# Kernel tuning notes

Hardware: AMD Instinct MI355X
Metric: run time of the kernel (lower is better)

Reference implementation:

```python
import jax, jax.numpy as jnp
import numpy as np

SEQ, N_NODES, N_EDGES = 64, 4096, 65536
IN_CH, HID, OUT = 128, 256, 256  # conv1: IN->2*HID, conv2: 2*HID->HID; HID==OUT required by the model


def setup_inputs() -> dict:
    key = jax.random.key(0)
    ks = jax.random.split(key, 10)
    s = 0.05
    return {
        "x": jax.random.normal(ks[0], (SEQ, N_NODES, IN_CH), jnp.float32),
        "edge_index": jax.random.randint(ks[1], (SEQ, 2, N_EDGES), 0, N_NODES),
        "W1l": jax.random.normal(ks[2], (IN_CH, 2 * HID), jnp.float32) * s,
        "b1l": jnp.zeros((2 * HID,), jnp.float32),
        "W1r": jax.random.normal(ks[3], (IN_CH, 2 * HID), jnp.float32) * s,
        "W2l": jax.random.normal(ks[4], (2 * HID, HID), jnp.float32) * s,
        "b2l": jnp.zeros((HID,), jnp.float32),
        "W2r": jax.random.normal(ks[5], (2 * HID, HID), jnp.float32) * s,
        "Wih": jax.random.normal(ks[6], (3 * OUT, HID), jnp.float32) * s,
        "Whh": jax.random.normal(ks[7], (3 * OUT, OUT), jnp.float32) * s,
        "bih": jnp.zeros((3 * OUT,), jnp.float32),
        "bhh": jnp.zeros((3 * OUT,), jnp.float32),
        "timestamp": 4,
        "n_samples": 8,
    }


def _sage(xt, src, dst, Wl, bl, Wr):
    # PyG SAGEConv: lin_l(mean-aggregated neighbor msgs) + lin_r(x); bias on lin_l only
    agg = jax.ops.segment_sum(xt[src], dst, num_segments=N_NODES)
    deg = jax.ops.segment_sum(jnp.ones((src.shape[0],), xt.dtype), dst, num_segments=N_NODES)
    agg = agg / jnp.maximum(deg, 1.0)[:, None]
    return agg @ Wl + bl + xt @ Wr


def _cpc_indices(seq_len, timestamp, n_samples):
    neg_dist = seq_len // 6
    end = seq_len - n_samples - neg_dist - timestamp + 2
    start = seq_len // 8 if seq_len // 8 < end else 0
    t_samples = np.arange(start, end)
    off = np.zeros((timestamp, n_samples), np.int32)
    for i in range(1, timestamp + 1):
        off[i - 1, 0] = i  # positive sample
        for j in range(1, n_samples):
            off[i - 1, j] = i + neg_dist + j - 1  # negatives
    return t_samples, off


def reference(x, edge_index, W1l, b1l, W1r, W2l, b2l, W2r, Wih, Whh, bih, bhh, timestamp, n_samples):
    def per_t(xt, ei):
        src, dst = ei[0], ei[1]
        h = jax.nn.relu(_sage(xt, src, dst, W1l, b1l, W1r))  # dropout(p=0.5) is identity in eval
        h = _sage(h, src, dst, W2l, b2l, W2r)
        return h.max(axis=0)  # global_max_pool over the single graph

    z = jax.vmap(per_t)(x, edge_index)  # [SEQ, HID]

    # torch GRU receives [1, t+1, H] seq-major => a single GRU-cell step per element, h0 = 0
    gi = z @ Wih.T + bih  # [SEQ, 3*OUT]
    r = jax.nn.sigmoid(gi[:, :OUT] + bhh[:OUT])
    u = jax.nn.sigmoid(gi[:, OUT:2 * OUT] + bhh[OUT:2 * OUT])
    n = jnp.tanh(gi[:, 2 * OUT:] + r * bhh[2 * OUT:])
    c = (1.0 - u) * n  # [SEQ, OUT] (Whh * h0 = 0)

    seq_len = z.shape[0]
    t_samples, off = _cpc_indices(seq_len, timestamp, n_samples)
    cnt = len(t_samples)
    idx = t_samples[:, None, None] + off[None]  # [T, timestamp, n_samples]
    enc = z[idx]  # [T, ts, ns, F]
    ct = c[t_samples]  # [T, F]

    eps = 1e-8  # torch cosine_similarity eps
    num = jnp.einsum('tijd,td->tij', enc, ct)
    den = jnp.maximum(jnp.linalg.norm(enc, axis=-1), eps) * \
          jnp.maximum(jnp.linalg.norm(ct, axis=-1), eps)[:, None, None]
    total = num / den  # [T, ts, ns]

    nce = -jax.nn.log_softmax(total, axis=-1)[..., 0].sum() / (cnt * timestamp)
    correct = (jnp.argmax(total, axis=-1) == 0).sum()  # softmax is monotone -> same argmax
    acc = correct / (cnt * timestamp)
    hidden = c[:t_samples[-1] + 1][None]  # GRU hidden of last loop iter: [1, t_last+1, OUT]
    return nce, acc, hidden
```

## Files before the change

kernel.cpp:

```cpp
#include <hip/hip_runtime.h>

#define T_SEQ 64
#define NV 4096
#define NE 65536
#define CIN 128
#define H2 512
#define HO 256
#define NEG_FLT (-3.402823466e38f)

typedef unsigned short u16;
typedef __bf16 bf16x8 __attribute__((ext_vector_type(8)));
typedef float f32x4 __attribute__((ext_vector_type(4)));

__device__ __forceinline__ u16 f2bf(float f){
  unsigned u = __float_as_uint(f);
  unsigned r = (u + 0x7FFFu + ((u >> 16) & 1u)) >> 16;
  return (u16)r;
}
__device__ __forceinline__ float bf2f(u16 h){
  return __uint_as_float(((unsigned)h) << 16);
}

__device__ __forceinline__ int swz8(){
  return (int)((blockIdx.x & 7) * (gridDim.x >> 3) + (blockIdx.x >> 3));
}

__device__ __forceinline__ void gll16(const u16* g, const uint4* l){
  __builtin_amdgcn_global_load_lds(
      reinterpret_cast<const __attribute__((address_space(1))) unsigned int*>(
          reinterpret_cast<uintptr_t>(g)),
      reinterpret_cast<__attribute__((address_space(3))) unsigned int*>(
          reinterpret_cast<uintptr_t>(l)),
      16, 0, 0);
}

#define WAITV(N) asm volatile("s_waitcnt vmcnt(" #N ")" ::: "memory")
#define BARRIER() do{ asm volatile("" ::: "memory"); \
                      __builtin_amdgcn_s_barrier(); \
                      asm volatile("" ::: "memory"); }while(0)

struct Lay {
  size_t z, c, zn, cn, Bt1h, Bt1l, Bt2h, Bt2l, cnt, fill, rowptr, deginv, csr,
         aggh, aggl, xh, xl, hh, hl, mh, partial, total;
};
static Lay mk_layout(int tc){
  Lay L; size_t o = 0;
  auto tk = [&](size_t b){ size_t p = o; o += ((b + 255) & ~(size_t)255); return p; };
  L.z       = tk((size_t)T_SEQ * HO * 4);
  L.c       = tk((size_t)T_SEQ * HO * 4);
  L.zn      = tk((size_t)T_SEQ * 4);
  L.cn      = tk((size_t)T_SEQ * 4);
  L.Bt1h    = tk((size_t)512 * 256 * 2);
  L.Bt1l    = tk((size_t)512 * 256 * 2);
  L.Bt2h    = tk((size_t)512 * 512 * 2);
  L.Bt2l    = tk((size_t)512 * 512 * 2);
  L.cnt     = tk((size_t)tc * NV * 4);
  L.fill    = tk((size_t)tc * NV * 4);
  L.rowptr  = tk((size_t)tc * (NV + 1) * 4);
  L.deginv  = tk((size_t)tc * NV * 4);
  L.csr     = tk((size_t)tc * NE * 4);
  L.aggh    = tk((size_t)tc * NV * CIN * 2);
  L.aggl    = tk((size_t)tc * NV * CIN * 2);
  L.xh      = tk((size_t)tc * NV * CIN * 2);
  L.xl      = tk((size_t)tc * NV * CIN * 2);
  L.hh      = tk((size_t)tc * NV * H2 * 2);
  L.hl      = tk((size_t)tc * NV * H2 * 2);
  L.mh      = tk((size_t)tc * NV * H2 * 4);
  L.partial = tk((size_t)tc * 128 * HO * 4);
  L.total = o; return L;
}

__global__ void k_init_out(float* out){
  int i = threadIdx.x;
  if (i < 2) out[i] = 0.0f;
}

__global__ void k_prep_Bt(const float* __restrict__ W1l, const float* __restrict__ W1r,
                          const float* __restrict__ W2l, const float* __restrict__ W2r,
                          u16* __restrict__ Bt1h, u16* __restrict__ Bt1l,
                          u16* __restrict__ Bt2h, u16* __restrict__ Bt2l){
  int i = blockIdx.x * 256 + threadIdx.x;
  if (i < 512 * 256){
    int n = i >> 8, k = i & 255;
    float v = (k < 128) ? W1l[k * 512 + n] : W1r[(k - 128) * 512 + n];
    u16 h = f2bf(v);
    Bt1h[i] = h; Bt1l[i] = f2bf(v - bf2f(h));
  } else {
    int j = i - 512 * 256;
    if (j < 512 * 512){
      int n = j >> 9, k = j & 511;
      float v = (n < 256) ? W2l[k * 256 + n] : W2r[k * 256 + (n - 256)];
      u16 h = f2bf(v);
      Bt2h[j] = h; Bt2l[j] = f2bf(v - bf2f(h));
    }
  }
}

__global__ void k_zero2(int* __restrict__ p, int* __restrict__ q, int n){
  int i = blockIdx.x * 256 + threadIdx.x;
  if (i < n){ p[i] = 0; q[i] = 0; }
}

__global__ void k_count(const int* __restrict__ ei, int t0, int tc, int* __restrict__ cnt){
  int i = blockIdx.x * 256 + threadIdx.x;
  if (i >= tc * NE) return;
  int tl = i >> 16, e = i & (NE - 1);
  int dst = ei[(size_t)(t0 + tl) * 2 * NE + NE + e];
  atomicAdd(&cnt[tl * NV + dst], 1);
}

__global__ void k_scan(const int* __restrict__ cnt, int* __restrict__ rowptr,
                       float* __restrict__ deginv){
  int tl = blockIdx.x, tid = threadIdx.x;
  __shared__ int s[256];
  int vals[16]; int sum = 0;
  const int* cb = cnt + tl * NV + tid * 16;
  #pragma unroll
  for (int i = 0; i < 16; i++){ vals[i] = cb[i]; sum += vals[i]; }
  s[tid] = sum; __syncthreads();
  for (int off = 1; off < 256; off <<= 1){
    int v = (tid >= off) ? s[tid - off] : 0;
    __syncthreads();
    s[tid] += v;
    __syncthreads();
  }
  int ex = s[tid] - sum;
  int* rp = rowptr + tl * (NV + 1) + tid * 16;
  float* dv = deginv + tl * NV + tid * 16;
  #pragma unroll
  for (int i = 0; i < 16; i++){
    rp[i] = ex; ex += vals[i];
    int d = vals[i] < 1 ? 1 : vals[i];
    dv[i] = 1.0f / (float)d;
  }
  if (tid == 255) rowptr[tl * (NV + 1) + NV] = ex;
}

__global__ void k_fill(const int* __restrict__ ei, int t0, int tc,
                       const int* __restrict__ rowptr, int* __restrict__ fill,
                       int* __restrict__ csr){
  int i = blockIdx.x * 256 + threadIdx.x;
  if (i >= tc * NE) return;
  int tl = i >> 16, e = i & (NE - 1);
  const int* eit = ei + (size_t)(t0 + tl) * 2 * NE;
  int src = eit[e], dst = eit[NE + e];
  int pos = atomicAdd(&fill[tl * NV + dst], 1);
  csr[tl * NE + rowptr[tl * (NV + 1) + dst] + pos] = src;
}

__global__ __launch_bounds__(256) void k_agg1(const float* __restrict__ x, int t0, int tc,
                       const int* __restrict__ rowptr, const int* __restrict__ csr,
                       const float* __restrict__ deginv,
                       u16* __restrict__ aggh, u16* __restrict__ aggl,
                       u16* __restrict__ xh, u16* __restrict__ xl){
  int bid = swz8();
  int w = (bid * 256 + threadIdx.x) >> 6;
  int lane = threadIdx.x & 63;
  if (w >= tc * NV) return;
  int tl = w >> 12, v = w & (NV - 1);
  const float2* xt = (const float2*)(x + (size_t)(t0 + tl) * NV * CIN);
  int beg = rowptr[tl * (NV + 1) + v], end = rowptr[tl * (NV + 1) + v + 1];
  const int* cs = csr + tl * NE;
  float ax = 0.f, ay = 0.f;
  int j = beg;
  for (; j + 1 < end; j += 2){
    int s0 = cs[j], s1 = cs[j + 1];
    float2 x0 = xt[(size_t)s0 * 64 + lane];
    float2 x1 = xt[(size_t)s1 * 64 + lane];
    ax += x0.x + x1.x; ay += x0.y + x1.y;
  }
  if (j < end){
    int s0 = cs[j];
    float2 x0 = xt[(size_t)s0 * 64 + lane];
    ax += x0.x; ay += x0.y;
  }
  float di = deginv[tl * NV + v];
  float vx = ax * di, vy = ay * di;
  u16 hx = f2bf(vx), hy = f2bf(vy);
  u16 lx = f2bf(vx - bf2f(hx)), ly = f2bf(vy - bf2f(hy));
  ushort2 hv; hv.x = hx; hv.y = hy;
  ushort2 lv; lv.x = lx; lv.y = ly;
  ((ushort2*)aggh)[(size_t)w * 64 + lane] = hv;
  ((ushort2*)aggl)[(size_t)w * 64 + lane] = lv;
  float2 xv = xt[(size_t)v * 64 + lane];
  u16 xhx = f2bf(xv.x), xhy = f2bf(xv.y);
  u16 xlx = f2bf(xv.x - bf2f(xhx)), xly = f2bf(xv.y - bf2f(xhy));
  ushort2 av; av.x = xhx; av.y = xhy;
  ushort2 bv; bv.x = xlx; bv.y = xly;
  ((ushort2*)xh)[(size_t)w * 64 + lane] = av;
  ((ushort2*)xl)[(size_t)w * 64 + lane] = bv;
}

__global__ __launch_bounds__(256, 2) void k_gemm_mfma(
    const u16* __restrict__ Ah0, const u16* __restrict__ Al0,
    const u16* __restrict__ Ah1, const u16* __restrict__ Al1,
    int ksplit, int lda,
    const u16* __restrict__ Bh, const u16* __restrict__ Bl, int K,
    const float* __restrict__ bias, int mode,
    u16* __restrict__ OutH, u16* __restrict__ OutL, float* __restrict__ OutF)
{
  __shared__ uint4 lds[4096];
  int tid = threadIdx.x;
  int bid = swz8();
  int bm = bid >> 2, bn = bid & 3;
  size_t row0 = (size_t)bm * 128;
  int col0 = bn * 128;
  int lane = tid & 63, wid = tid >> 6;
  int wm = wid >> 1, wn = wid & 1;
  int l15 = lane & 15, l4 = lane >> 4;

  size_t aoff[2], boff[2];
  int cslot[2];
  #pragma unroll
  for (int q = 0; q < 2; q++){
    int c = 2 * wid + q;
    aoff[q] = (row0 + c * 16 + l15) * (size_t)lda + (size_t)(l4 * 8);
    boff[q] = (size_t)(col0 + c * 16 + l15) * K + (size_t)(l4 * 8);
    cslot[q] = c * 64;
  }

#define STAGE(T) do { \
    int kk0_ = (T) << 5; \
    const u16* pAh_ = Ah0; const u16* pAl_ = Al0; int kA_ = kk0_; \
    if (kk0_ >= ksplit){ pAh_ = Ah1; pAl_ = Al1; kA_ = kk0_ - ksplit; } \
    int bb_ = ((T) & 1) << 11; \
    _Pragma("unroll") \
    for (int q = 0; q < 2; q++){ \
      gll16(pAh_ + aoff[q] + kA_, &lds[bb_ + cslot[q]]); \
      gll16(pAl_ + aoff[q] + kA_, &lds[bb_ + 512 + cslot[q]]); \
      gll16(Bh + boff[q] + kk0_, &lds[bb_ + 1024 + cslot[q]]); \
      gll16(Bl + boff[q] + kk0_, &lds[bb_ + 1536 + cslot[q]]); \
    } \
  } while (0)

  f32x4 zv = {0.f, 0.f, 0.f, 0.f};
  f32x4 acc[4][4];
  #pragma unroll
  for (int i = 0; i < 4; i++)
    #pragma unroll
    for (int j = 0; j < 4; j++) acc[i][j] = zv;

  STAGE(0);

  int nt = K >> 5;
  for (int t = 0; t < nt; t++){
    if (t + 1 < nt){ STAGE(t + 1); WAITV(8); }
    else          { WAITV(0); }
    BARRIER();
    int base = (t & 1) << 11;
    int abase = base + wm * 256;
    int bbase = base + 1024 + wn * 256;
    bf16x8 ah[4], al[4], bh[4], bl[4];
    #pragma unroll
    for (int f = 0; f < 4; f++){
      ah[f] = __builtin_bit_cast(bf16x8, lds[abase + f * 64 + lane]);
      al[f] = __builtin_bit_cast(bf16x8, lds[abase + 512 + f * 64 + lane]);
      bh[f] = __builtin_bit_cast(bf16x8, lds[bbase + f * 64 + lane]);
      bl[f] = __builtin_bit_cast(bf16x8, lds[bbase + 512 + f * 64 + lane]);
    }
    #pragma unroll
    for (int i = 0; i < 4; i++)
      #pragma unroll
      for (int j = 0; j < 4; j++){
        acc[i][j] = __builtin_amdgcn_mfma_f32_16x16x32_bf16(ah[i], bh[j], acc[i][j], 0, 0, 0);
        acc[i][j] = __builtin_amdgcn_mfma_f32_16x16x32_bf16(ah[i], bl[j], acc[i][j], 0, 0, 0);
        acc[i][j] = __builtin_amdgcn_mfma_f32_16x16x32_bf16(al[i], bh[j], acc[i][j], 0, 0, 0);
      }
    BARRIER();
  }
#undef STAGE

  #pragma unroll
  for (int i = 0; i < 4; i++){
    #pragma unroll
    for (int j = 0; j < 4; j++){
      int col = col0 + wn * 64 + j * 16 + l15;
      float bv = bias ? bias[col] : 0.f;
      #pragma unroll
      for (int r = 0; r < 4; r++){
        size_t row = row0 + wm * 64 + i * 16 + l4 * 4 + r;
        float v = acc[i][j][r] + bv;
        if (mode == 1){
          v = fmaxf(v, 0.f);
          u16 h = f2bf(v);
          u16 l = f2bf(v - bf2f(h));
          OutH[row * 512 + col] = h;
          OutL[row * 512 + col] = l;
        } else {
          OutF[row * 512 + col] = v;
        }
      }
    }
  }
}

__global__ __launch_bounds__(256) void k_conv2agg(
    const float* __restrict__ mh, const int* __restrict__ rowptr,
    const int* __restrict__ csr, const float* __restrict__ deginv,
    const float* __restrict__ b2l, float* __restrict__ partial){
  int blk = swz8();
  int tl = blk >> 7, nb = blk & 127;
  int wid = threadIdx.x >> 6, lane = threadIdx.x & 63;
  const float4* m4 = (const float4*)mh;
  const int* rp = rowptr + tl * (NV + 1);
  const int* cs = csr + tl * NE;
  size_t tB = (size_t)tl * NV;
  float4 bb = ((const float4*)b2l)[lane];
  float4 vmax; vmax.x = NEG_FLT; vmax.y = NEG_FLT; vmax.z = NEG_FLT; vmax.w = NEG_FLT;
  int v0 = nb * 32 + wid * 8;
  for (int q = 0; q < 8; q++){
    int v = v0 + q;
    int beg = rp[v], end = rp[v + 1];
    float4 acc; acc.x = 0.f; acc.y = 0.f; acc.z = 0.f; acc.w = 0.f;
    int j = beg;
    for (; j + 1 < end; j += 2){
      int s0 = cs[j], s1 = cs[j + 1];
      float4 a0 = m4[(tB + s0) * 128 + lane];
      float4 a1 = m4[(tB + s1) * 128 + lane];
      acc.x += a0.x + a1.x; acc.y += a0.y + a1.y;
      acc.z += a0.z + a1.z; acc.w += a0.w + a1.w;
    }
    if (j < end){
      int s0 = cs[j];
      float4 a0 = m4[(tB + s0) * 128 + lane];
      acc.x += a0.x; acc.y += a0.y; acc.z += a0.z; acc.w += a0.w;
    }
    float di = deginv[tl * NV + v];
    float4 hr = m4[(tB + v) * 128 + 64 + lane];
    float4 val;
    val.x = acc.x * di + bb.x + hr.x;
    val.y = acc.y * di + bb.y + hr.y;
    val.z = acc.z * di + bb.z + hr.z;
    val.w = acc.w * di + bb.w + hr.w;
    vmax.x = fmaxf(vmax.x, val.x); vmax.y = fmaxf(vmax.y, val.y);
    vmax.z = fmaxf(vmax.z, val.z); vmax.w = fmaxf(vmax.w, val.w);
  }
  __shared__ float4 sm[4][64];
  sm[wid][lane] = vmax;
  __syncthreads();
  if (wid == 0){
    float4 a = sm[0][lane], b = sm[1][lane], c = sm[2][lane], d = sm[3][lane];
    float4 r;
    r.x = fmaxf(fmaxf(a.x, b.x), fmaxf(c.x, d.x));
    r.y = fmaxf(fmaxf(a.y, b.y), fmaxf(c.y, d.y));
    r.z = fmaxf(fmaxf(a.z, b.z), fmaxf(c.z, d.z));
    r.w = fmaxf(fmaxf(a.w, b.w), fmaxf(c.w, d.w));
    ((float4*)partial)[((size_t)(tl * 128 + nb)) * 64 + lane] = r;
  }
}

__global__ void k_pool(const float* __restrict__ partial, int t0,
                       float* __restrict__ z){
  int blk = blockIdx.x;
  int tl = blk >> 2, cg = blk & 3;
  int tid = threadIdx.x;
  int c = cg * 64 + (tid & 63);
  int grp = tid >> 6;
  float m = NEG_FLT;
  for (int b = grp; b < 128; b += 4)
    m = fmaxf(m, partial[((size_t)(tl * 128 + b)) * HO + c]);
  __shared__ float s[4][64];
  s[grp][tid & 63] = m;
  __syncthreads();
  if (grp == 0){
    m = fmaxf(fmaxf(s[0][tid], s[1][tid]), fmaxf(s[2][tid], s[3][tid]));
    z[(t0 + tl) * HO + c] = m;
  }
}

__global__ void k_gru(const float* __restrict__ z, const float* __restrict__ Wih,
                      const float* __restrict__ bih, const float* __restrict__ bhh,
                      float* __restrict__ c, float* __restrict__ cn, float* __restrict__ out){
  int s0 = blockIdx.x, j = threadIdx.x;
  __shared__ float zs[256];
  __shared__ float ss[256];
  zs[j] = z[s0 * HO + j];
  __syncthreads();
  const float* wr = Wih + (size_t)j * HO;
  const float* wu = Wih + (size_t)(HO + j) * HO;
  const float* wn = Wih + (size_t)(2 * HO + j) * HO;
  float gr = bih[j], gu = bih[HO + j], gn = bih[2 * HO + j];
  for (int k = 0; k < HO; k++){
    float zv = zs[k];
    gr = fmaf(zv, wr[k], gr);
    gu = fmaf(zv, wu[k], gu);
    gn = fmaf(zv, wn[k], gn);
  }
  float r = 1.f / (1.f + expf(-(gr + bhh[j])));
  float u = 1.f / (1.f + expf(-(gu + bhh[HO + j])));
  float n = tanhf(gn + r * bhh[2 * HO + j]);
  float cv = (1.f - u) * n;
  c[s0 * HO + j] = cv;
  if (s0 < 44) out[2 + s0 * HO + j] = cv;
  ss[j] = cv * cv; __syncthreads();
  for (int off = 128; off > 0; off >>= 1){
    if (j < off) ss[j] += ss[j + off];
    __syncthreads();
  }
  if (j == 0) cn[s0] = sqrtf(ss[0]);
}

__global__ void k_cpc(const float* __restrict__ z, const float* __restrict__ c,
                      const float* __restrict__ cn, float* __restrict__ out){
  int tt = blockIdx.x;
  int ts = 8 + tt;
  int tid = threadIdx.x;
  __shared__ float ct[256];
  __shared__ float tot[32];
  ct[tid] = c[ts * HO + tid];
  __syncthreads();
  int g = tid >> 3, r = tid & 7;
  int i = g >> 3, j = g & 7;
  int idx = ts + ((j == 0) ? (i + 1) : (i + j + 10));
  const float* zr = z + idx * HO;
  float s = 0.f, nz = 0.f;
  for (int k = r; k < HO; k += 8){
    float zv = zr[k];
    s = fmaf(zv, ct[k], s);
    nz = fmaf(zv, zv, nz);
  }
  s += __shfl_down(s, 4, 8);  nz += __shfl_down(nz, 4, 8);
  s += __shfl_down(s, 2, 8);  nz += __shfl_down(nz, 2, 8);
  s += __shfl_down(s, 1, 8);  nz += __shfl_down(nz, 1, 8);
  if (r == 0){
    float den = fmaxf(sqrtf(nz), 1e-8f) * fmaxf(cn[ts], 1e-8f);
    tot[g] = s / den;
  }
  __syncthreads();
  if (tid < 4){
    const float* tr = tot + tid * 8;
    float m = tr[0];
    for (int q = 1; q < 8; q++) m = fmaxf(m, tr[q]);
    float se = 0.f;
    for (int q = 0; q < 8; q++) se += expf(tr[q] - m);
    float lse = m + logf(se);
    float nce = (lse - tr[0]) * (1.0f / 144.0f);
    float corr = (tr[0] == m) ? (1.0f / 144.0f) : 0.f;
    atomicAdd(&out[0], nce);
    atomicAdd(&out[1], corr);
  }
}

extern "C" void kernel_launch(void* const* d_in, const int* in_sizes, int n_in,
                              void* d_out, int out_size, void* d_ws, size_t ws_size,
                              hipStream_t stream){
  const float* x   = (const float*)d_in[0];
  const int*   ei  = (const int*)  d_in[1];
  const float* W1l = (const float*)d_in[2];
  const float* b1l = (const float*)d_in[3];
  const float* W1r = (const float*)d_in[4];
  const float* W2l = (const float*)d_in[5];
  const float* b2l = (const float*)d_in[6];
  const float* W2r = (const float*)d_in[7];
  const float* Wih = (const float*)d_in[8];
  const float* bih = (const float*)d_in[10];
  const float* bhh = (const float*)d_in[11];
  float* out = (float*)d_out;

  int tc = 64;
  while (tc > 1 && mk_layout(tc).total > ws_size) tc >>= 1;
  Lay L = mk_layout(tc);
  char* w = (char*)d_ws;
  float* zB   = (float*)(w + L.z);
  float* cB   = (float*)(w + L.c);
  float* cnB  = (float*)(w + L.cn);
  u16*   Bt1h = (u16*)  (w + L.Bt1h);
  u16*   Bt1l = (u16*)  (w + L.Bt1l);
  u16*   Bt2h = (u16*)  (w + L.Bt2h);
  u16*   Bt2l = (u16*)  (w + L.Bt2l);
  int*   cnt  = (int*)  (w + L.cnt);
  int*   fill = (int*)  (w + L.fill);
  int*   rp   = (int*)  (w + L.rowptr);
  float* dinv = (float*)(w + L.deginv);
  int*   csr  = (int*)  (w + L.csr);
  u16*   aggh = (u16*)  (w + L.aggh);
  u16*   aggl = (u16*)  (w + L.aggl);
  u16*   xh   = (u16*)  (w + L.xh);
  u16*   xl   = (u16*)  (w + L.xl);
  u16*   hh   = (u16*)  (w + L.hh);
  u16*   hl   = (u16*)  (w + L.hl);
  float* mhB  = (float*)(w + L.mh);
  float* part = (float*)(w + L.partial);

  hipLaunchKernelGGL(k_init_out, dim3(1), dim3(64), 0, stream, out);
  hipLaunchKernelGGL(k_prep_Bt, dim3(1536), dim3(256), 0, stream,
                     W1l, W1r, W2l, W2r, Bt1h, Bt1l, Bt2h, Bt2l);

  for (int t0 = 0; t0 < T_SEQ; t0 += tc){
    int nE = tc * NE;
    int M = tc * NV;
    hipLaunchKernelGGL(k_zero2, dim3((tc * NV + 255) / 256), dim3(256), 0, stream,
                       cnt, fill, tc * NV);
    hipLaunchKernelGGL(k_count, dim3((nE + 255) / 256), dim3(256), 0, stream, ei, t0, tc, cnt);
    hipLaunchKernelGGL(k_scan, dim3(tc), dim3(256), 0, stream, cnt, rp, dinv);
    hipLaunchKernelGGL(k_fill, dim3((nE + 255) / 256), dim3(256), 0, stream, ei, t0, tc, rp, fill, csr);
    hipLaunchKernelGGL(k_agg1, dim3(tc * NV / 4), dim3(256), 0, stream,
                       x, t0, tc, rp, csr, dinv, aggh, aggl, xh, xl);
    hipLaunchKernelGGL(k_gemm_mfma, dim3((M / 128) * 4), dim3(256), 0, stream,
                       aggh, aggl, xh, xl, 128, CIN,
                       Bt1h, Bt1l, 256, b1l, 1, hh, hl, (float*)nullptr);
    hipLaunchKernelGGL(k_gemm_mfma, dim3((M / 128) * 4), dim3(256), 0, stream,
                       hh, hl, hh, hl, 1 << 30, H2,
                       Bt2h, Bt2l, 512, (const float*)nullptr, 0,
                       (u16*)nullptr, (u16*)nullptr, mhB);
    hipLaunchKernelGGL(k_conv2agg, dim3(tc * 128), dim3(256), 0, stream,
                       mhB, rp, csr, dinv, b2l, part);
    hipLaunchKernelGGL(k_pool, dim3(tc * 4), dim3(256), 0, stream, part, t0, zB);
  }

  hipLaunchKernelGGL(k_gru, dim3(T_SEQ), dim3(256), 0, stream, zB, Wih, bih, bhh, cB, cnB, out);
  hipLaunchKernelGGL(k_cpc, dim3(36), dim3(256), 0, stream, zB, cB, cnB, out);
  (void)in_sizes; (void)n_in; (void)out_size;
}
```

Before: 2.301 ms.

## Replace LDS-staged GEMM tiles with direct register double-buffered global loads

The split-bf16 MFMA GEMM no longer stages A/B tiles through LDS with global_load_lds and barriers. Each wave now loads its own 16x8 fragments straight from global memory into two register buffers and alternates them across K steps, with MFMAs grouped by hi/lo product and wrapped in s_setprio. This drops LDS traffic and barrier stalls, but each wave fetches its own copy of the shared A/B data, so global/L2 traffic rises and register pressure grows with four 8-entry uint4 buffers.

```diff
diff --git a/kernel.cpp b/kernel.cpp
--- a/kernel.cpp
+++ b/kernel.cpp
@@ -24,20 +24,6 @@
 __device__ __forceinline__ int swz8(){
   return (int)((blockIdx.x & 7) * (gridDim.x >> 3) + (blockIdx.x >> 3));
 }
-
-__device__ __forceinline__ void gll16(const u16* g, const uint4* l){
-  __builtin_amdgcn_global_load_lds(
-      reinterpret_cast<const __attribute__((address_space(1))) unsigned int*>(
-          reinterpret_cast<uintptr_t>(g)),
-      reinterpret_cast<__attribute__((address_space(3))) unsigned int*>(
-          reinterpret_cast<uintptr_t>(l)),
-      16, 0, 0);
-}
-
-#define WAITV(N) asm volatile("s_waitcnt vmcnt(" #N ")" ::: "memory")
-#define BARRIER() do{ asm volatile("" ::: "memory"); \
-                      __builtin_amdgcn_s_barrier(); \
-                      asm volatile("" ::: "memory"); }while(0)
 
 struct Lay {
   size_t z, c, zn, cn, Bt1h, Bt1l, Bt2h, Bt2l, cnt, fill, rowptr, deginv, csr,
@@ -199,7 +185,6 @@
     const float* __restrict__ bias, int mode,
     u16* __restrict__ OutH, u16* __restrict__ OutL, float* __restrict__ OutF)
 {
-  __shared__ uint4 lds[4096];
   int tid = threadIdx.x;
   int bid = swz8();
   int bm = bid >> 2, bn = bid & 3;
@@ -209,28 +194,50 @@
   int wm = wid >> 1, wn = wid & 1;
   int l15 = lane & 15, l4 = lane >> 4;
 
-  size_t aoff[2], boff[2];
-  int cslot[2];
+  unsigned aoff[4], boff[4];
   #pragma unroll
-  for (int q = 0; q < 2; q++){
-    int c = 2 * wid + q;
-    aoff[q] = (row0 + c * 16 + l15) * (size_t)lda + (size_t)(l4 * 8);
-    boff[q] = (size_t)(col0 + c * 16 + l15) * K + (size_t)(l4 * 8);
-    cslot[q] = c * 64;
-  }
-
-#define STAGE(T) do { \
+  for (int i = 0; i < 4; i++){
+    aoff[i] = (unsigned)((row0 + wm * 64 + i * 16 + l15) * (unsigned)lda + l4 * 8);
+    boff[i] = (unsigned)((unsigned)(col0 + wn * 64 + i * 16 + l15) * (unsigned)K + l4 * 8);
+  }
+
+#define LOADF(RA, RB, T) do { \
     int kk0_ = (T) << 5; \
     const u16* pAh_ = Ah0; const u16* pAl_ = Al0; int kA_ = kk0_; \
     if (kk0_ >= ksplit){ pAh_ = Ah1; pAl_ = Al1; kA_ = kk0_ - ksplit; } \
-    int bb_ = ((T) & 1) << 11; \
     _Pragma("unroll") \
-    for (int q = 0; q < 2; q++){ \
-      gll16(pAh_ + aoff[q] + kA_, &lds[bb_ + cslot[q]]); \
-      gll16(pAl_ + aoff[q] + kA_, &lds[bb_ + 512 + cslot[q]]); \
-      gll16(Bh + boff[q] + kk0_, &lds[bb_ + 1024 + cslot[q]]); \
-      gll16(Bl + boff[q] + kk0_, &lds[bb_ + 1536 + cslot[q]]); \
+    for (int i_ = 0; i_ < 4; i_++){ \
+      RA[i_]     = *(const uint4*)(pAh_ + aoff[i_] + kA_); \
+      RA[i_ + 4] = *(const uint4*)(pAl_ + aoff[i_] + kA_); \
+      RB[i_]     = *(const uint4*)(Bh + boff[i_] + kk0_); \
+      RB[i_ + 4] = *(const uint4*)(Bl + boff[i_] + kk0_); \
     } \
+  } while (0)
+
+#define MFMAC(RA, RB) do { \
+    __builtin_amdgcn_s_setprio(1); \
+    _Pragma("unroll") \
+    for (int i_ = 0; i_ < 4; i_++) \
+      _Pragma("unroll") \
+      for (int j_ = 0; j_ < 4; j_++) \
+        acc[i_][j_] = __builtin_amdgcn_mfma_f32_16x16x32_bf16( \
+            __builtin_bit_cast(bf16x8, RA[i_]), __builtin_bit_cast(bf16x8, RB[j_]), \
+            acc[i_][j_], 0, 0, 0); \
+    _Pragma("unroll") \
+    for (int i_ = 0; i_ < 4; i_++) \
+      _Pragma("unroll") \
+      for (int j_ = 0; j_ < 4; j_++) \
+        acc[i_][j_] = __builtin_amdgcn_mfma_f32_16x16x32_bf16( \
+            __builtin_bit_cast(bf16x8, RA[i_]), __builtin_bit_cast(bf16x8, RB[j_ + 4]), \
+            acc[i_][j_], 0, 0, 0); \
+    _Pragma("unroll") \
+    for (int i_ = 0; i_ < 4; i_++) \
+      _Pragma("unroll") \
+      for (int j_ = 0; j_ < 4; j_++) \
+        acc[i_][j_] = __builtin_amdgcn_mfma_f32_16x16x32_bf16( \
+            __builtin_bit_cast(bf16x8, RA[i_ + 4]), __builtin_bit_cast(bf16x8, RB[j_]), \
+            acc[i_][j_], 0, 0, 0); \
+    __builtin_amdgcn_s_setprio(0); \
   } while (0)
 
   f32x4 zv = {0.f, 0.f, 0.f, 0.f};
@@ -240,35 +247,18 @@
     #pragma unroll
     for (int j = 0; j < 4; j++) acc[i][j] = zv;
 
-  STAGE(0);
+  uint4 A0r[8], B0r[8], A1r[8], B1r[8];
+  LOADF(A0r, B0r, 0);
 
   int nt = K >> 5;
-  for (int t = 0; t < nt; t++){
-    if (t + 1 < nt){ STAGE(t + 1); WAITV(8); }
-    else          { WAITV(0); }
-    BARRIER();
-    int base = (t & 1) << 11;
-    int abase = base + wm * 256;
-    int bbase = base + 1024 + wn * 256;
-    bf16x8 ah[4], al[4], bh[4], bl[4];
-    #pragma unroll
-    for (int f = 0; f < 4; f++){
-      ah[f] = __builtin_bit_cast(bf16x8, lds[abase + f * 64 + lane]);
-      al[f] = __builtin_bit_cast(bf16x8, lds[abase + 512 + f * 64 + lane]);
-      bh[f] = __builtin_bit_cast(bf16x8, lds[bbase + f * 64 + lane]);
-      bl[f] = __builtin_bit_cast(bf16x8, lds[bbase + 512 + f * 64 + lane]);
-    }
-    #pragma unroll
-    for (int i = 0; i < 4; i++)
-      #pragma unroll
-      for (int j = 0; j < 4; j++){
-        acc[i][j] = __builtin_amdgcn_mfma_f32_16x16x32_bf16(ah[i], bh[j], acc[i][j], 0, 0, 0);
-        acc[i][j] = __builtin_amdgcn_mfma_f32_16x16x32_bf16(ah[i], bl[j], acc[i][j], 0, 0, 0);
-        acc[i][j] = __builtin_amdgcn_mfma_f32_16x16x32_bf16(al[i], bh[j], acc[i][j], 0, 0, 0);
-      }
-    BARRIER();
-  }
-#undef STAGE
+  for (int t = 0; t < nt; t += 2){
+    LOADF(A1r, B1r, t + 1);
+    MFMAC(A0r, B0r);
+    if (t + 2 < nt) LOADF(A0r, B0r, t + 2);
+    MFMAC(A1r, B1r);
+  }
+#undef LOADF
+#undef MFMAC
 
   #pragma unroll
   for (int i = 0; i < 4; i++){
```

After: 2.846 ms. 1.24x slower.
